# Kernel optimization log

Hardware: AMD Instinct MI355X
Metric: run time of the kernel (lower is better)

The kernel has to match this reference:

```python
import jax, jax.numpy as jnp
import numpy as np

B, LAT, MEM, IMG = 8192, 256, 200, 128
THRESHOLD = 1.0 / MEM          # sparse-addressing threshold 1/MEM_DIM
EPS_SHRINK = 1e-12             # module epsilon
EPS_COS = 1e-8                 # torch CosineSimilarity default eps
EPS_L1 = 1e-12                 # torch F.normalize default eps


def setup_inputs() -> dict:
    key = jax.random.key(0)
    k1, k2, k3 = jax.random.split(key, 3)
    z = jax.random.normal(k1, (B, LAT), dtype=jnp.float32)          # encoder latent
    memory = jax.random.normal(k2, (MEM, LAT), dtype=jnp.float32) * 0.05  # kaiming-scale memory
    W = jax.random.normal(k3, (IMG * IMG, LAT), dtype=jnp.float32) * 0.02  # linear weight
    b = jnp.zeros((IMG * IMG,), dtype=jnp.float32)
    return {"z": z, "memory": memory, "W": W, "b": b}


def reference(z, memory, W, b):
    # Cosine similarity via normalized matmul (no [B,MEM,LAT] repeat tensors)
    zn = jnp.linalg.norm(z, axis=1, keepdims=True)          # [B,1]
    mn = jnp.linalg.norm(memory, axis=1, keepdims=True)     # [MEM,1]
    logits = (z @ memory.T) / jnp.maximum(zn * mn.T, EPS_COS)  # [B,MEM]
    w = jax.nn.softmax(logits, axis=1)
    # sparse shrinkage: relu(w-t)*w/(|w-t|+eps)
    w = jax.nn.relu(w - THRESHOLD) * w / (jnp.abs(w - THRESHOLD) + EPS_SHRINK)
    # L1 normalize over memory dim
    w = w / jnp.maximum(jnp.sum(jnp.abs(w), axis=1, keepdims=True), EPS_L1)
    z_hat = w @ memory                                      # [B,LAT]
    x_hat = (z_hat @ W.T + b).reshape(-1, 1, IMG, IMG)      # [B,1,128,128]
    return x_hat, z_hat, w
```

## Files before the change

kernel.cpp:

```cpp
#include <hip/hip_runtime.h>
#include <hip/hip_bf16.h>
#include <stdint.h>

#define B_DIM   8192
#define LAT     256
#define MEM_DIM 200
#define MEM_PAD 208
#define MEMT_K  224
#define MEMT_S  232
#define NPIX    16384
#define RPB     16

typedef short bf16x8 __attribute__((ext_vector_type(8)));
typedef float f32x4  __attribute__((ext_vector_type(4)));

__device__ __forceinline__ float wred_sum(float v) {
#pragma unroll
  for (int m = 32; m; m >>= 1) v += __shfl_xor(v, m, 64);
  return v;
}
__device__ __forceinline__ float wred_max(float v) {
#pragma unroll
  for (int m = 32; m; m >>= 1) v = fmaxf(v, __shfl_xor(v, m, 64));
  return v;
}
__device__ __forceinline__ unsigned short f2bf(float f) {
  unsigned u = __builtin_bit_cast(unsigned, f);
  u = u + 0x7FFFu + ((u >> 16) & 1u);
  return (unsigned short)(u >> 16);
}
__device__ __forceinline__ float bf2f(unsigned short h) {
  return __builtin_bit_cast(float, (unsigned)h << 16);
}
__device__ __forceinline__ void split3(float v, unsigned short& h, unsigned short& m,
                                       unsigned short& l) {
  h = f2bf(v);
  float r1 = v - bf2f(h);
  m = f2bf(r1);
  float r2 = r1 - bf2f(m);
  l = f2bf(r2);
}

__global__ void __launch_bounds__(64) mem_norm_kernel(
    const float* __restrict__ mem, float* __restrict__ mn,
    unsigned short* __restrict__ mem_h, unsigned short* __restrict__ mem_m,
    unsigned short* __restrict__ mem_l,
    unsigned short* __restrict__ memT_h, unsigned short* __restrict__ memT_m,
    unsigned short* __restrict__ memT_l) {
  const int m = blockIdx.x, lane = threadIdx.x;
  if (m >= MEM_DIM) {
    ushort4 zz = {0, 0, 0, 0};
    if (m < MEM_PAD) {
      ((ushort4*)(mem_h + (size_t)m * LAT))[lane] = zz;
      ((ushort4*)(mem_m + (size_t)m * LAT))[lane] = zz;
      ((ushort4*)(mem_l + (size_t)m * LAT))[lane] = zz;
    }
#pragma unroll
    for (int q = 0; q < 4; ++q) {
      const size_t o = (size_t)(lane * 4 + q) * MEMT_S + m;
      memT_h[o] = 0; memT_m[o] = 0; memT_l[o] = 0;
    }
    return;
  }
  float4 v = ((const float4*)(mem + (size_t)m * LAT))[lane];
  ushort4 h, md, l;
  split3(v.x, h.x, md.x, l.x); split3(v.y, h.y, md.y, l.y);
  split3(v.z, h.z, md.z, l.z); split3(v.w, h.w, md.w, l.w);
  ((ushort4*)(mem_h + (size_t)m * LAT))[lane] = h;
  ((ushort4*)(mem_m + (size_t)m * LAT))[lane] = md;
  ((ushort4*)(mem_l + (size_t)m * LAT))[lane] = l;
  const float vv[4] = {v.x, v.y, v.z, v.w};
#pragma unroll
  for (int q = 0; q < 4; ++q) {
    unsigned short th, tm, tl;
    split3(vv[q], th, tm, tl);
    const size_t o = (size_t)(lane * 4 + q) * MEMT_S + m;
    memT_h[o] = th; memT_m[o] = tm; memT_l[o] = tl;
  }
  float ss = v.x * v.x + v.y * v.y + v.z * v.z + v.w * v.w;
  ss = wred_sum(ss);
  if (lane == 0) mn[m] = sqrtf(ss);
}

__global__ void __launch_bounds__(256) zsplit_kernel(const float* __restrict__ z,
                                                     unsigned short* __restrict__ z_h,
                                                     unsigned short* __restrict__ z_m,
                                                     unsigned short* __restrict__ z_l) {
  const int i = blockIdx.x * 256 + threadIdx.x;
  float4 v = ((const float4*)z)[i];
  ushort4 h, md, l;
  split3(v.x, h.x, md.x, l.x); split3(v.y, h.y, md.y, l.y);
  split3(v.z, h.z, md.z, l.z); split3(v.w, h.w, md.w, l.w);
  ((ushort4*)z_h)[i] = h;
  ((ushort4*)z_m)[i] = md;
  ((ushort4*)z_l)[i] = l;
}

__global__ void __launch_bounds__(256) convert_w_kernel(const float* __restrict__ W,
                                                        unsigned short* __restrict__ Wb) {
  const int i = blockIdx.x * 256 + threadIdx.x;
  float4 v = ((const float4*)W)[i];
  ushort4 o;
  o.x = f2bf(v.x); o.y = f2bf(v.y); o.z = f2bf(v.z); o.w = f2bf(v.w);
  ((ushort4*)Wb)[i] = o;
}

__global__ void __launch_bounds__(256) row_kernel(
    const float* __restrict__ z, const float* __restrict__ mn_g,
    const unsigned short* __restrict__ z_h, const unsigned short* __restrict__ z_m,
    const unsigned short* __restrict__ z_l,
    const unsigned short* __restrict__ mem_h, const unsigned short* __restrict__ mem_m,
    const unsigned short* __restrict__ mem_l,
    const unsigned short* __restrict__ memT_h, const unsigned short* __restrict__ memT_m,
    const unsigned short* __restrict__ memT_l,
    float* __restrict__ zhat_out, float* __restrict__ w_out,
    unsigned short* __restrict__ zhat_bf) {
  __shared__ float lw[RPB][MEM_DIM];
  __shared__ float mnsh[MEM_DIM];
  __shared__ unsigned short whsh[16 * MEMT_S];
  __shared__ unsigned short wmsh[16 * MEMT_S];
  __shared__ unsigned short wlsh[16 * MEMT_S];

  const int tid = threadIdx.x;
  const int lane = tid & 63;
  const int wid = tid >> 6;
  const int row0 = blockIdx.x * RPB;
  const int fr_ = lane & 15;
  const int kq8 = (lane >> 4) * 8;

  if (tid < MEM_DIM) mnsh[tid] = mn_g[tid];

  float zn[4];
#pragma unroll
  for (int r = 0; r < 4; ++r) {
    const int row = row0 + wid * 4 + r;
    float4 zr = *(const float4*)(z + (size_t)row * LAT + lane * 4);
    float ss = zr.x * zr.x + zr.y * zr.y + zr.z * zr.z + zr.w * zr.w;
    zn[r] = sqrtf(wred_sum(ss));
  }

  {
    const size_t zoff = (size_t)(row0 + fr_) * LAT + kq8;
    const unsigned short* zh_p = z_h + zoff;
    const unsigned short* zm_p = z_m + zoff;
    const unsigned short* zl_p = z_l + zoff;
    for (int nf = wid; nf <= 12; nf += 4) {
      const size_t moff = (size_t)(nf * 16 + fr_) * LAT + kq8;
      const unsigned short* mh_p = mem_h + moff;
      const unsigned short* mm_p = mem_m + moff;
      const unsigned short* ml_p = mem_l + moff;
      f32x4 a = {};
#pragma unroll
      for (int kk = 0; kk < 8; ++kk) {
        bf16x8 zh = *(const bf16x8*)(zh_p + kk * 32);
        bf16x8 zm = *(const bf16x8*)(zm_p + kk * 32);
        bf16x8 zl = *(const bf16x8*)(zl_p + kk * 32);
        bf16x8 mh = *(const bf16x8*)(mh_p + kk * 32);
        bf16x8 mm = *(const bf16x8*)(mm_p + kk * 32);
        bf16x8 ml = *(const bf16x8*)(ml_p + kk * 32);
        a = __builtin_amdgcn_mfma_f32_16x16x32_bf16(zm, mm, a, 0, 0, 0);
        a = __builtin_amdgcn_mfma_f32_16x16x32_bf16(zh, ml, a, 0, 0, 0);
        a = __builtin_amdgcn_mfma_f32_16x16x32_bf16(zl, mh, a, 0, 0, 0);
        a = __builtin_amdgcn_mfma_f32_16x16x32_bf16(zm, mh, a, 0, 0, 0);
        a = __builtin_amdgcn_mfma_f32_16x16x32_bf16(zh, mm, a, 0, 0, 0);
        a = __builtin_amdgcn_mfma_f32_16x16x32_bf16(zh, mh, a, 0, 0, 0);
      }
      const int m = nf * 16 + fr_;
      if (m < MEM_DIM) {
#pragma unroll
        for (int q = 0; q < 4; ++q)
          lw[(lane >> 4) * 4 + q][m] = a[q];
      }
    }
  }
  __syncthreads();

  const float t = 0.005f;
#pragma unroll
  for (int r = 0; r < 4; ++r) {
    const int lr = wid * 4 + r;
    float lg[4];
#pragma unroll
    for (int i = 0; i < 4; ++i) {
      const int m = lane + 64 * i;
      lg[i] = (m < MEM_DIM) ? lw[lr][m] / fmaxf(zn[r] * mnsh[m], 1e-8f) : -1e30f;
    }
    float mx = wred_max(fmaxf(fmaxf(lg[0], lg[1]), fmaxf(lg[2], lg[3])));
    float e[4]; float s = 0.f;
#pragma unroll
    for (int i = 0; i < 4; ++i) {
      const int m = lane + 64 * i;
      e[i] = (m < MEM_DIM) ? expf(lg[i] - mx) : 0.f;
      s += e[i];
    }
    s = wred_sum(s);
    float sv[4]; float l1 = 0.f;
#pragma unroll
    for (int i = 0; i < 4; ++i) {
      const float wv = e[i] / s;
      const float d = wv - t;
      sv[i] = fmaxf(d, 0.f) * wv / (fabsf(d) + 1e-12f);
      l1 += sv[i];
    }
    l1 = wred_sum(l1);
    const float dnm = fmaxf(l1, 1e-12f);
#pragma unroll
    for (int i = 0; i < 4; ++i) {
      const int m = lane + 64 * i;
      if (m < MEM_DIM) {
        const float wn = sv[i] / dnm;
        lw[lr][m] = wn;
        w_out[(size_t)(row0 + lr) * MEM_DIM + m] = wn;
      }
    }
  }
  __syncthreads();

  for (int idx = tid; idx < 16 * MEMT_S; idx += 256) {
    const int lr = idx / MEMT_S, m = idx % MEMT_S;
    const float val = (m < MEM_DIM) ? lw[lr][m] : 0.f;
    unsigned short h, md, l;
    split3(val, h, md, l);
    whsh[idx] = h; wmsh[idx] = md; wlsh[idx] = l;
  }
  __syncthreads();

  {
    f32x4 zacc[4] = {};
    for (int kk = 0; kk < 7; ++kk) {
      const int ko = kk * 32 + kq8;
      bf16x8 wh = *(const bf16x8*)&whsh[fr_ * MEMT_S + ko];
      bf16x8 wm = *(const bf16x8*)&wmsh[fr_ * MEMT_S + ko];
      bf16x8 wl = *(const bf16x8*)&wlsh[fr_ * MEMT_S + ko];
#pragma unroll
      for (int nf = 0; nf < 4; ++nf) {
        const size_t mo = (size_t)(wid * 64 + nf * 16 + fr_) * MEMT_S + ko;
        bf16x8 th = *(const bf16x8*)(memT_h + mo);
        bf16x8 tm = *(const bf16x8*)(memT_m + mo);
        bf16x8 tl = *(const bf16x8*)(memT_l + mo);
        zacc[nf] = __builtin_amdgcn_mfma_f32_16x16x32_bf16(tm, wm, zacc[nf], 0, 0, 0);
        zacc[nf] = __builtin_amdgcn_mfma_f32_16x16x32_bf16(th, wl, zacc[nf], 0, 0, 0);
        zacc[nf] = __builtin_amdgcn_mfma_f32_16x16x32_bf16(tl, wh, zacc[nf], 0, 0, 0);
        zacc[nf] = __builtin_amdgcn_mfma_f32_16x16x32_bf16(tm, wh, zacc[nf], 0, 0, 0);
        zacc[nf] = __builtin_amdgcn_mfma_f32_16x16x32_bf16(th, wm, zacc[nf], 0, 0, 0);
        zacc[nf] = __builtin_amdgcn_mfma_f32_16x16x32_bf16(th, wh, zacc[nf], 0, 0, 0);
      }
    }
    const size_t orow = (size_t)(row0 + fr_) * LAT;
#pragma unroll
    for (int nf = 0; nf < 4; ++nf) {
      const int d0 = wid * 64 + nf * 16 + (lane >> 4) * 4;
      float4 o;
      o.x = zacc[nf][0]; o.y = zacc[nf][1]; o.z = zacc[nf][2]; o.w = zacc[nf][3];
      *(float4*)(zhat_out + orow + d0) = o;
      ushort4 ob;
      ob.x = f2bf(o.x); ob.y = f2bf(o.y); ob.z = f2bf(o.z); ob.w = f2bf(o.w);
      *(ushort4*)(zhat_bf + orow + d0) = ob;
    }
  }
}

#define STAGE(bufbase, t)                                                      \
  {                                                                            \
    const int k0_ = (t) * 32;                                                  \
    _Pragma("unroll")                                                          \
    for (int cc = 0; cc < 2; ++cc) {                                           \
      const int r_ = r0 + cc * 16;                                             \
      __builtin_amdgcn_global_load_lds(                                        \
          (const __attribute__((address_space(1))) void*)(const void*)         \
              (A + (size_t)(brow + r_) * LAT + k0_ + kq),                      \
          (__attribute__((address_space(3))) void*)(void*)                     \
              &smem[(bufbase) + (ch0 + cc) * 1024], 16, 0, 0);                 \
      __builtin_amdgcn_global_load_lds(                                        \
          (const __attribute__((address_space(1))) void*)(const void*)         \
              (Bw + (size_t)(bcol + r_) * LAT + k0_ + kq),                     \
          (__attribute__((address_space(3))) void*)(void*)                     \
              &smem[(bufbase) + 8192 + (ch0 + cc) * 1024], 16, 0, 0);          \
    }                                                                          \
  }

#define GEMM_PROLOG_AND_KLOOP                                                  \
  const int tid = threadIdx.x;                                                 \
  const int lane = tid & 63;                                                   \
  const int wid = tid >> 6;                                                    \
  const int swz = (blockIdx.x & 7) * 1024 + (blockIdx.x >> 3);                 \
  const int st = swz >> 8;                                                     \
  const int loc = swz & 255;                                                   \
  const int tm = (st >> 3) * 16 + (loc & 15);                                  \
  const int tn = (st & 7) * 16 + (loc >> 4);                                   \
  const int brow = tm * 128;                                                   \
  const int bcol = tn * 128;                                                   \
  const int wr = wid >> 1, wc = wid & 1;                                       \
  const int ch0 = wid * 2;                                                     \
  const int r0 = ch0 * 16 + (lane >> 2);                                       \
  const int kq = (lane & 3) * 8;                                               \
  f32x4 acc[4][4] = {};                                                        \
  STAGE(0, 0);                                                                 \
  STAGE(16384, 1);                                                             \
  STAGE(32768, 2);                                                             \
  _Pragma("unroll")                                                            \
  for (int t = 0; t < 8; ++t) {                                                \
    if (t < 6)       asm volatile("s_waitcnt vmcnt(8)" ::: "memory");          \
    else if (t == 6) asm volatile("s_waitcnt vmcnt(4)" ::: "memory");          \
    else             asm volatile("s_waitcnt vmcnt(0)" ::: "memory");          \
    __builtin_amdgcn_sched_barrier(0);                                         \
    __builtin_amdgcn_s_barrier();                                              \
    const int bufb = (t % 3) * 16384;                                          \
    bf16x8 af[4], bfr[4];                                                      \
    _Pragma("unroll")                                                          \
    for (int mf = 0; mf < 4; ++mf)                                             \
      af[mf] = *(const bf16x8*)&smem[bufb + (wr * 64 + mf * 16 + (lane & 15)) * 64 + (lane >> 4) * 16]; \
    _Pragma("unroll")                                                          \
    for (int nf = 0; nf < 4; ++nf)                                             \
      bfr[nf] = *(const bf16x8*)&smem[bufb + 8192 + (wc * 64 + nf * 16 + (lane & 15)) * 64 + (lane >> 4) * 16]; \
    asm volatile("s_waitcnt lgkmcnt(0)" ::: "memory");                         \
    __builtin_amdgcn_sched_barrier(0);                                         \
    __builtin_amdgcn_s_barrier();                                              \
    if (t + 3 < 8) STAGE(((t + 3) % 3) * 16384, t + 3);                        \
    _Pragma("unroll")                                                          \
    for (int mf = 0; mf < 4; ++mf)                                             \
      _Pragma("unroll")                                                        \
      for (int nf = 0; nf < 4; ++nf)                                           \
        acc[mf][nf] = __builtin_amdgcn_mfma_f32_16x16x32_bf16(af[mf], bfr[nf], acc[mf][nf], 0, 0, 0); \
  }

#define TSTRIDE 68
__global__ void __launch_bounds__(256, 3) gemm_xhat_kernel(
    const unsigned short* __restrict__ A, const unsigned short* __restrict__ Bw,
    const float* __restrict__ bias, float* __restrict__ C) {
  __shared__ __align__(16) unsigned char smem[49152];

  if (blockIdx.x < 768) {
    const int d = blockIdx.x >> 8;
    for (int i = 0; i < d; ++i) {
#pragma unroll
      for (int s = 0; s < 8; ++s)
        __builtin_amdgcn_s_sleep(100);
    }
  }

  GEMM_PROLOG_AND_KLOOP

  __syncthreads();
  float* tt = (float*)(smem + wid * (16 * TSTRIDE * 4));

  const int colq = (lane & 15) * 4;
  const int col0 = bcol + wc * 64 + colq;
  const float4 bv4 = *(const float4*)(bias + col0);

#pragma unroll
  for (int mf = 0; mf < 4; ++mf) {
#pragma unroll
    for (int nf = 0; nf < 4; ++nf) {
      const int cl = nf * 16 + (lane & 15);
#pragma unroll
      for (int q = 0; q < 4; ++q)
        tt[((lane >> 4) * 4 + q) * TSTRIDE + cl] = acc[mf][nf][q];
    }
#pragma unroll
    for (int rr = 0; rr < 4; ++rr) {
      const int rl = rr * 4 + (lane >> 4);
      float4 v = *(const float4*)&tt[rl * TSTRIDE + colq];
      f32x4 ve;
      ve[0] = v.x + bv4.x; ve[1] = v.y + bv4.y;
      ve[2] = v.z + bv4.z; ve[3] = v.w + bv4.w;
      const int row = brow + wr * 64 + mf * 16 + rl;
      __builtin_nontemporal_store(ve, (f32x4*)&C[(size_t)row * NPIX + col0]);
    }
  }
}

extern "C" void kernel_launch(void* const* d_in, const int* in_sizes, int n_in,
                              void* d_out, int out_size, void* d_ws, size_t ws_size,
                              hipStream_t stream) {
  const float* z    = (const float*)d_in[0];
  const float* mem  = (const float*)d_in[1];
  const float* W    = (const float*)d_in[2];
  const float* bias = (const float*)d_in[3];

  float* xhat = (float*)d_out;
  float* zhat = xhat + (size_t)B_DIM * NPIX;
  float* wout = zhat + (size_t)B_DIM * LAT;

  unsigned short* z_h    = (unsigned short*)xhat;
  unsigned short* z_m    = z_h + (size_t)B_DIM * LAT;
  unsigned short* z_l    = z_m + (size_t)B_DIM * LAT;
  unsigned short* mem_h  = z_l + (size_t)B_DIM * LAT;
  unsigned short* mem_m  = mem_h + (size_t)MEM_PAD * LAT;
  unsigned short* mem_l  = mem_m + (size_t)MEM_PAD * LAT;
  unsigned short* memT_h = mem_l + (size_t)MEM_PAD * LAT;
  unsigned short* memT_m = memT_h + (size_t)256 * MEMT_S;
  unsigned short* memT_l = memT_m + (size_t)256 * MEMT_S;

  unsigned short* Wb  = (unsigned short*)d_ws;
  unsigned short* zhb = Wb + (size_t)NPIX * LAT;
  float* mn = (float*)(zhb + (size_t)B_DIM * LAT);

  mem_norm_kernel<<<MEMT_K, 64, 0, stream>>>(mem, mn, mem_h, mem_m, mem_l,
                                             memT_h, memT_m, memT_l);
  zsplit_kernel<<<(B_DIM * LAT / 4) / 256, 256, 0, stream>>>(z, z_h, z_m, z_l);
  convert_w_kernel<<<(NPIX * LAT / 4) / 256, 256, 0, stream>>>(W, Wb);
  row_kernel<<<B_DIM / RPB, 256, 0, stream>>>(z, mn, z_h, z_m, z_l,
                                              mem_h, mem_m, mem_l,
                                              memT_h, memT_m, memT_l,
                                              zhat, wout, zhb);
  gemm_xhat_kernel<<<8192, 256, 0, stream>>>(zhb, Wb, bias, xhat);
}
```

Before: 217.3 us.

## Merge prep kernels, halve row_kernel rows per block, drop GEMM stagger sleeps

Fuses the z split and W bf16 conversion into a single prep kernel, saving one launch. Halves the rows per block in row_kernel to 8, launching twice as many blocks for more parallelism at the cost of wasting half of each 16-row MFMA tile. Removes the s_sleep staggering at the start of the first GEMM blocks. Each change is independent and touches a different stage.

```diff
diff --git a/kernel.cpp b/kernel.cpp
--- a/kernel.cpp
+++ b/kernel.cpp
@@ -9,7 +9,9 @@
 #define MEMT_K  224
 #define MEMT_S  232
 #define NPIX    16384
-#define RPB     16
+#define RPB     8
+#define W_QUADS (NPIX * LAT / 4)
+#define Z_QUADS (B_DIM * LAT / 4)
 
 typedef short bf16x8 __attribute__((ext_vector_type(8)));
 typedef float f32x4  __attribute__((ext_vector_type(4)));
@@ -82,27 +84,26 @@
   if (lane == 0) mn[m] = sqrtf(ss);
 }
 
-__global__ void __launch_bounds__(256) zsplit_kernel(const float* __restrict__ z,
-                                                     unsigned short* __restrict__ z_h,
-                                                     unsigned short* __restrict__ z_m,
-                                                     unsigned short* __restrict__ z_l) {
+__global__ void __launch_bounds__(256) prep_kernel(
+    const float* __restrict__ W, unsigned short* __restrict__ Wb,
+    const float* __restrict__ z, unsigned short* __restrict__ z_h,
+    unsigned short* __restrict__ z_m, unsigned short* __restrict__ z_l) {
   const int i = blockIdx.x * 256 + threadIdx.x;
-  float4 v = ((const float4*)z)[i];
-  ushort4 h, md, l;
-  split3(v.x, h.x, md.x, l.x); split3(v.y, h.y, md.y, l.y);
-  split3(v.z, h.z, md.z, l.z); split3(v.w, h.w, md.w, l.w);
-  ((ushort4*)z_h)[i] = h;
-  ((ushort4*)z_m)[i] = md;
-  ((ushort4*)z_l)[i] = l;
-}
-
-__global__ void __launch_bounds__(256) convert_w_kernel(const float* __restrict__ W,
-                                                        unsigned short* __restrict__ Wb) {
-  const int i = blockIdx.x * 256 + threadIdx.x;
-  float4 v = ((const float4*)W)[i];
-  ushort4 o;
-  o.x = f2bf(v.x); o.y = f2bf(v.y); o.z = f2bf(v.z); o.w = f2bf(v.w);
-  ((ushort4*)Wb)[i] = o;
+  if (i < W_QUADS) {
+    float4 v = ((const float4*)W)[i];
+    ushort4 o;
+    o.x = f2bf(v.x); o.y = f2bf(v.y); o.z = f2bf(v.z); o.w = f2bf(v.w);
+    ((ushort4*)Wb)[i] = o;
+  } else {
+    const int j = i - W_QUADS;
+    float4 v = ((const float4*)z)[j];
+    ushort4 h, md, l;
+    split3(v.x, h.x, md.x, l.x); split3(v.y, h.y, md.y, l.y);
+    split3(v.z, h.z, md.z, l.z); split3(v.w, h.w, md.w, l.w);
+    ((ushort4*)z_h)[j] = h;
+    ((ushort4*)z_m)[j] = md;
+    ((ushort4*)z_l)[j] = l;
+  }
 }
 
 __global__ void __launch_bounds__(256) row_kernel(
@@ -130,17 +131,17 @@
 
   if (tid < MEM_DIM) mnsh[tid] = mn_g[tid];
 
-  float zn[4];
-#pragma unroll
-  for (int r = 0; r < 4; ++r) {
-    const int row = row0 + wid * 4 + r;
+  float zn[2];
+#pragma unroll
+  for (int r = 0; r < 2; ++r) {
+    const int row = row0 + wid * 2 + r;
     float4 zr = *(const float4*)(z + (size_t)row * LAT + lane * 4);
     float ss = zr.x * zr.x + zr.y * zr.y + zr.z * zr.z + zr.w * zr.w;
     zn[r] = sqrtf(wred_sum(ss));
   }
 
   {
-    const size_t zoff = (size_t)(row0 + fr_) * LAT + kq8;
+    const size_t zoff = (size_t)(row0 + (fr_ & 7)) * LAT + kq8;
     const unsigned short* zh_p = z_h + zoff;
     const unsigned short* zm_p = z_m + zoff;
     const unsigned short* zl_p = z_l + zoff;
@@ -166,7 +167,7 @@
         a = __builtin_amdgcn_mfma_f32_16x16x32_bf16(zh, mh, a, 0, 0, 0);
       }
       const int m = nf * 16 + fr_;
-      if (m < MEM_DIM) {
+      if (m < MEM_DIM && lane < 32) {
 #pragma unroll
         for (int q = 0; q < 4; ++q)
           lw[(lane >> 4) * 4 + q][m] = a[q];
@@ -177,8 +178,8 @@
 
   const float t = 0.005f;
 #pragma unroll
-  for (int r = 0; r < 4; ++r) {
-    const int lr = wid * 4 + r;
+  for (int r = 0; r < 2; ++r) {
+    const int lr = wid * 2 + r;
     float lg[4];
 #pragma unroll
     for (int i = 0; i < 4; ++i) {
@@ -218,7 +219,7 @@
 
   for (int idx = tid; idx < 16 * MEMT_S; idx += 256) {
     const int lr = idx / MEMT_S, m = idx % MEMT_S;
-    const float val = (m < MEM_DIM) ? lw[lr][m] : 0.f;
+    const float val = (lr < RPB && m < MEM_DIM) ? lw[lr][m] : 0.f;
     unsigned short h, md, l;
     split3(val, h, md, l);
     whsh[idx] = h; wmsh[idx] = md; wlsh[idx] = l;
@@ -246,16 +247,18 @@
         zacc[nf] = __builtin_amdgcn_mfma_f32_16x16x32_bf16(th, wh, zacc[nf], 0, 0, 0);
       }
     }
-    const size_t orow = (size_t)(row0 + fr_) * LAT;
-#pragma unroll
-    for (int nf = 0; nf < 4; ++nf) {
-      const int d0 = wid * 64 + nf * 16 + (lane >> 4) * 4;
-      float4 o;
-      o.x = zacc[nf][0]; o.y = zacc[nf][1]; o.z = zacc[nf][2]; o.w = zacc[nf][3];
-      *(float4*)(zhat_out + orow + d0) = o;
-      ushort4 ob;
-      ob.x = f2bf(o.x); ob.y = f2bf(o.y); ob.z = f2bf(o.z); ob.w = f2bf(o.w);
-      *(ushort4*)(zhat_bf + orow + d0) = ob;
+    if (fr_ < RPB) {
+      const size_t orow = (size_t)(row0 + fr_) * LAT;
+#pragma unroll
+      for (int nf = 0; nf < 4; ++nf) {
+        const int d0 = wid * 64 + nf * 16 + (lane >> 4) * 4;
+        float4 o;
+        o.x = zacc[nf][0]; o.y = zacc[nf][1]; o.z = zacc[nf][2]; o.w = zacc[nf][3];
+        *(float4*)(zhat_out + orow + d0) = o;
+        ushort4 ob;
+        ob.x = f2bf(o.x); ob.y = f2bf(o.y); ob.z = f2bf(o.z); ob.w = f2bf(o.w);
+        *(ushort4*)(zhat_bf + orow + d0) = ob;
+      }
     }
   }
 }
@@ -330,15 +333,6 @@
     const float* __restrict__ bias, float* __restrict__ C) {
   __shared__ __align__(16) unsigned char smem[49152];
 
-  if (blockIdx.x < 768) {
-    const int d = blockIdx.x >> 8;
-    for (int i = 0; i < d; ++i) {
-#pragma unroll
-      for (int s = 0; s < 8; ++s)
-        __builtin_amdgcn_s_sleep(100);
-    }
-  }
-
   GEMM_PROLOG_AND_KLOOP
 
   __syncthreads();
@@ -398,8 +392,7 @@
 
   mem_norm_kernel<<<MEMT_K, 64, 0, stream>>>(mem, mn, mem_h, mem_m, mem_l,
                                              memT_h, memT_m, memT_l);
-  zsplit_kernel<<<(B_DIM * LAT / 4) / 256, 256, 0, stream>>>(z, z_h, z_m, z_l);
-  convert_w_kernel<<<(NPIX * LAT / 4) / 256, 256, 0, stream>>>(W, Wb);
+  prep_kernel<<<(W_QUADS + Z_QUADS) / 256, 256, 0, stream>>>(W, Wb, z, z_h, z_m, z_l);
   row_kernel<<<B_DIM / RPB, 256, 0, stream>>>(z, mn, z_h, z_m, z_l,
                                               mem_h, mem_m, mem_l,
                                               memT_h, memT_m, memT_l,
```

After: 234.3 us. 1.08x slower.
